# Kernel tuning notes

Measured on AMD Instinct MI355X. Metric: run time of the kernel, lower is better.

## Reference

```python
import jax, jax.numpy as jnp
import numpy as np

C = 64
C2 = C // 2


def conv1x1(x, w, b):
    # x: [B,Cin,H,W], w: [Cout,Cin], b: [Cout]
    return jnp.einsum('bchw,oc->bohw', x, w) + b[None, :, None, None]


def maxpool2(x):
    # 2x2 max pool, stride 2. x: [B,C,H,W] -> [B,C,H//2,W//2]
    B, Ch, H, W = x.shape
    x = x.reshape(B, Ch, H // 2, 2, W // 2, 2)
    return x.max(axis=(3, 5))


def setup_inputs() -> dict:
    key = jax.random.key(0)
    ks = jax.random.split(key, 9)
    B, H, W = 4, 128, 128
    x = jax.random.normal(ks[0], (B, C, H, W), dtype=jnp.float32)
    s_in = 1.0 / np.sqrt(C)
    s_mid = 1.0 / np.sqrt(C2)
    return {
        'x': x,
        'w_theta': jax.random.uniform(ks[1], (C2, C), jnp.float32, -s_in, s_in),
        'b_theta': jax.random.uniform(ks[2], (C2,), jnp.float32, -s_in, s_in),
        'w_phi': jax.random.uniform(ks[3], (C2, C), jnp.float32, -s_in, s_in),
        'b_phi': jax.random.uniform(ks[4], (C2,), jnp.float32, -s_in, s_in),
        'w_g': jax.random.uniform(ks[5], (C2, C), jnp.float32, -s_in, s_in),
        'b_g': jax.random.uniform(ks[6], (C2,), jnp.float32, -s_in, s_in),
        'w_out': jax.random.uniform(ks[7], (C, C2), jnp.float32, -s_mid, s_mid),
        'b_out': jax.random.uniform(ks[8], (C,), jnp.float32, -s_mid, s_mid),
    }


def reference(x, w_theta, b_theta, w_phi, b_phi, w_g, b_g, w_out, b_out):
    B, Ch, H, W = x.shape
    theta = conv1x1(x, w_theta, b_theta)            # [B,C2,H,W]
    phi = maxpool2(conv1x1(x, w_phi, b_phi))        # [B,C2,H/2,W/2]
    g = maxpool2(conv1x1(x, w_g, b_g))              # [B,C2,H/2,W/2]

    theta_flat = theta.reshape(B, C2, H * W).transpose(0, 2, 1)   # [B,HW,C2]
    phi_flat = phi.reshape(B, C2, -1)                              # [B,C2,hw4]
    g_flat = g.reshape(B, C2, -1).transpose(0, 2, 1)               # [B,hw4,C2]

    attn = jnp.einsum('bnc,bcm->bnm', theta_flat, phi_flat)       # [B,HW,hw4]
    attn = jax.nn.softmax(attn, axis=-1)
    y = jnp.einsum('bnm,bmc->bnc', attn, g_flat)                   # [B,HW,C2]
    y = y.transpose(0, 2, 1).reshape(B, C2, H, W)
    return conv1x1(y, w_out, b_out) + x
```

## Files before the change

kernel.cpp:

```cpp
#include <hip/hip_runtime.h>

#define HW    16384
#define Wh    128
#define Cin   64
#define C2    32
#define HW4   4096

typedef short short8 __attribute__((ext_vector_type(8)));
typedef float float4v __attribute__((ext_vector_type(4)));
typedef unsigned uint4v __attribute__((ext_vector_type(4)));

#define LOG2E 1.44269504f
#define OFFE  43.2808512f

__device__ __forceinline__ unsigned pack2bf16(float lo, float hi) {
  unsigned ul = __builtin_bit_cast(unsigned, lo);
  unsigned uh = __builtin_bit_cast(unsigned, hi);
  ul = (ul + 0x7fffu + ((ul >> 16) & 1u)) >> 16;
  uh = (uh + 0x7fffu + ((uh >> 16) & 1u)) & 0xffff0000u;
  return ul | uh;
}
__device__ __forceinline__ unsigned short f2bf(float f) {
  unsigned u = __builtin_bit_cast(unsigned, f);
  return (unsigned short)((u + 0x7fffu + ((u >> 16) & 1u)) >> 16);
}
__device__ __forceinline__ unsigned packtrunc(float lo, float hi) {
  return __builtin_amdgcn_perm(__builtin_bit_cast(unsigned, hi),
                               __builtin_bit_cast(unsigned, lo), 0x07060302u);
}

__global__ __launch_bounds__(256) void repack_w_kern(
    const float* __restrict__ wt, const float* __restrict__ bt,
    const float* __restrict__ wp, const float* __restrict__ bp,
    const float* __restrict__ wg, const float* __restrict__ bg,
    float* __restrict__ wAll, float* __restrict__ bAll) {
  int idx = blockIdx.x * 256 + threadIdx.x;
  if (idx < 6144) {
    int og = idx / 1536, rem = idx % 1536;
    int c = rem / 24, j = rem % 24;
    int o = og * 8 + (j & 7);
    float v;
    if (j < 8)       v = wt[o * Cin + c] * LOG2E;
    else if (j < 16) v = wp[o * Cin + c];
    else             v = wg[o * Cin + c];
    wAll[idx] = v;
  } else if (idx < 6240) {
    int i2 = idx - 6144;
    int og = i2 / 24, j = i2 % 24;
    int o = og * 8 + (j & 7);
    bAll[i2] = (j < 8) ? bt[o] * LOG2E : (j < 16 ? bp[o] : bg[o]);
  }
}

__global__ __launch_bounds__(256) void conv_qkv_kern(
    const float* __restrict__ x, const float* __restrict__ wAll,
    const float* __restrict__ bAll, unsigned short* __restrict__ Q,
    unsigned short* __restrict__ K, unsigned short* __restrict__ Vt) {
  __shared__ float smX[2][8][256];
  __shared__ unsigned short smV[8][64];
  int tid = threadIdx.x;
  int og = blockIdx.y, bz = blockIdx.z;
  int pxbase = blockIdx.x * 2 * Wh;
  int jloc = tid >> 2;
  int rpar = (tid >> 1) & 1, cpar = tid & 1;
  int myPx = rpar * Wh + 2 * jloc + cpar;
  const float* xb = x + (size_t)bz * Cin * HW + pxbase;
  const float* wc = wAll + og * 1536;
  const float* bb = bAll + og * 24;

  auto stage = [&](int cb8, int buf) {
#pragma unroll
    for (int u = 0; u < 2; ++u) {
      int f = u * 256 + tid;
      int ch = f >> 6, p4 = f & 63;
      *(float4*)&smX[buf][ch][p4 * 4] =
          *(const float4*)(xb + (size_t)(cb8 * 8 + ch) * HW + p4 * 4);
    }
  };

  float acc[24];
#pragma unroll
  for (int k = 0; k < 24; ++k) acc[k] = bb[k];

  stage(0, 0);
  __syncthreads();
  for (int cb8 = 0; cb8 < 8; ++cb8) {
    if (cb8 < 7) stage(cb8 + 1, (cb8 + 1) & 1);
    float xv[8];
#pragma unroll
    for (int u = 0; u < 8; ++u) xv[u] = smX[cb8 & 1][u][myPx];
#pragma unroll
    for (int u = 0; u < 8; ++u) {
#pragma unroll
      for (int k = 0; k < 24; ++k)
        acc[k] = fmaf(wc[(cb8 * 8 + u) * 24 + k], xv[u], acc[k]);
    }
    __syncthreads();
  }

  int pp = blockIdx.x * 64 + jloc;
  int p = pxbase + myPx;
  {
    uint4 up;
    up.x = pack2bf16(acc[0], acc[1]); up.y = pack2bf16(acc[2], acc[3]);
    up.z = pack2bf16(acc[4], acc[5]); up.w = pack2bf16(acc[6], acc[7]);
    *(uint4*)(Q + ((size_t)bz * HW + p) * C2 + og * 8) = up;
  }
  float aP[8], aG[8];
#pragma unroll
  for (int o = 0; o < 8; ++o) {
    float vp = acc[8 + o], vg = acc[16 + o];
    vp = fmaxf(vp, __shfl_xor(vp, 1)); vp = fmaxf(vp, __shfl_xor(vp, 2));
    vg = fmaxf(vg, __shfl_xor(vg, 1)); vg = fmaxf(vg, __shfl_xor(vg, 2));
    aP[o] = vp; aG[o] = vg;
  }
  if ((tid & 3) == 0) {
    int loc = pp & 31, tile = pp >> 5;
    int prow = ((loc & 4) << 2) + ((loc >> 3) << 2) + (loc & 3);
    uint4 up;
    up.x = pack2bf16(aP[0], aP[1]); up.y = pack2bf16(aP[2], aP[3]);
    up.z = pack2bf16(aP[4], aP[5]); up.w = pack2bf16(aP[6], aP[7]);
    *(uint4*)(K + ((size_t)bz * HW4 + tile * 32 + prow) * C2 + og * 8) = up;
#pragma unroll
    for (int o = 0; o < 8; ++o) smV[o][tid >> 2] = f2bf(aG[o]);
  }
  __syncthreads();
  {
    int ch = tid >> 5, idx = tid & 31;
    unsigned v = ((unsigned*)smV)[ch * 32 + idx];
    *(unsigned*)(Vt + (size_t)bz * C2 * HW4 + (size_t)(og * 8 + ch) * HW4 +
                 blockIdx.x * 64 + 2 * idx) = v;
  }
}

__global__ __launch_bounds__(256, 4) void attn_mfma_kern(
    const unsigned short* __restrict__ Qb, const unsigned short* __restrict__ Kb,
    const unsigned short* __restrict__ Vt, const float* __restrict__ x,
    const float* __restrict__ w_out, const float* __restrict__ b_out,
    float* __restrict__ out) {
  __shared__ float smY[3][64][33];
  __shared__ float smL[4][64];
  int lane = threadIdx.x & 63;
  int wv = threadIdx.x >> 6;
  int quad = lane >> 4, l16 = lane & 15;
  int bz = blockIdx.y;
  int qrow0 = blockIdx.x * 64;

  short8 qf[4];
#pragma unroll
  for (int f = 0; f < 4; ++f)
    qf[f] = *(const short8*)(Qb + ((size_t)bz * HW + qrow0 + f * 16 + l16) * C2 + quad * 8);
  const unsigned short* kb = Kb + ((size_t)bz * HW4 + wv * 1024) * C2;
  const unsigned short* vb = Vt + (size_t)bz * C2 * HW4 + wv * 1024;

  short8 ones;
#pragma unroll
  for (int i = 0; i < 8; ++i) ones[i] = (short)0x3F80;

  float4v z = {0.f, 0.f, 0.f, 0.f};
  float4v ya[4] = {z, z, z, z};
  float4v yh[4] = {z, z, z, z};
  float4v y2[4] = {z, z, z, z};
  float4v moff = {-OFFE, -OFFE, -OFFE, -OFFE};

  for (int t = 0; t < 32; ++t) {
    const unsigned short* kt = kb + (size_t)t * 32 * C2;
    const unsigned short* vt = vb + t * 32;
    short8 ka = *(const short8*)(kt + (size_t)l16 * C2 + quad * 8);
    short8 kh = *(const short8*)(kt + (size_t)(16 + l16) * C2 + quad * 8);
    short8 va = *(const short8*)(vt + (size_t)l16 * HW4 + quad * 8);
    short8 vh = *(const short8*)(vt + (size_t)(16 + l16) * HW4 + quad * 8);
#pragma unroll
    for (int f = 0; f < 4; ++f) {
      float4v sa = __builtin_amdgcn_mfma_f32_16x16x32_bf16(ka, qf[f], moff, 0, 0, 0);
      float4v sh = __builtin_amdgcn_mfma_f32_16x16x32_bf16(kh, qf[f], moff, 0, 0, 0);
      float e0 = __builtin_amdgcn_exp2f(sa[0]), e1 = __builtin_amdgcn_exp2f(sa[1]);
      float e2 = __builtin_amdgcn_exp2f(sa[2]), e3 = __builtin_amdgcn_exp2f(sa[3]);
      float g0 = __builtin_amdgcn_exp2f(sh[0]), g1 = __builtin_amdgcn_exp2f(sh[1]);
      float g2 = __builtin_amdgcn_exp2f(sh[2]), g3 = __builtin_amdgcn_exp2f(sh[3]);
      uint4v d = {packtrunc(e0, e1), packtrunc(e2, e3),
                  packtrunc(g0, g1), packtrunc(g2, g3)};
      short8 pf = __builtin_bit_cast(short8, d);
      ya[f] = __builtin_amdgcn_mfma_f32_16x16x32_bf16(pf, va,   ya[f], 0, 0, 0);
      yh[f] = __builtin_amdgcn_mfma_f32_16x16x32_bf16(pf, vh,   yh[f], 0, 0, 0);
      y2[f] = __builtin_amdgcn_mfma_f32_16x16x32_bf16(pf, ones, y2[f], 0, 0, 0);
    }
  }

  if (l16 == 0) {
#pragma unroll
    for (int f = 0; f < 4; ++f)
#pragma unroll
      for (int r = 0; r < 4; ++r)
        smL[wv][f * 16 + quad * 4 + r] = y2[f][r];
  }
  if (wv > 0) {
    int pi = wv - 1;
#pragma unroll
    for (int f = 0; f < 4; ++f)
#pragma unroll
      for (int r = 0; r < 4; ++r) {
        int lr = f * 16 + quad * 4 + r;
        smY[pi][lr][l16] = ya[f][r];
        smY[pi][lr][16 + l16] = yh[f][r];
      }
  }
  __syncthreads();
  if (wv == 0) {
#pragma unroll
    for (int f = 0; f < 4; ++f)
#pragma unroll
      for (int r = 0; r < 4; ++r) {
        int lr = f * 16 + quad * 4 + r;
        float a0 = ya[f][r] + smY[0][lr][l16] + smY[1][lr][l16] + smY[2][lr][l16];
        float a1 = yh[f][r] + smY[0][lr][16 + l16] + smY[1][lr][16 + l16] + smY[2][lr][16 + l16];
        float L = smL[0][lr] + smL[1][lr] + smL[2][lr] + smL[3][lr];
        float inv = 1.f / L;
        smY[0][lr][l16] = a0 * inv;
        smY[0][lr][16 + l16] = a1 * inv;
      }
  }
  __syncthreads();

  {
    int px = lane;
    float yv[C2];
#pragma unroll
    for (int c = 0; c < C2; ++c) yv[c] = smY[0][px][c];
    const float* xb = x + (size_t)bz * Cin * HW + qrow0 + px;
    float* ob = out + (size_t)bz * Cin * HW + qrow0 + px;
#pragma unroll
    for (int i = 0; i < 16; ++i) {
      int co = wv * 16 + i;
      float s = b_out[co];
#pragma unroll
      for (int o = 0; o < C2; ++o) s = fmaf(w_out[co * C2 + o], yv[o], s);
      ob[(size_t)co * HW] = s + xb[(size_t)co * HW];
    }
  }
}

extern "C" void kernel_launch(void* const* d_in, const int* in_sizes, int n_in,
                              void* d_out, int out_size, void* d_ws, size_t ws_size,
                              hipStream_t stream) {
  const float* x       = (const float*)d_in[0];
  const float* w_theta = (const float*)d_in[1];
  const float* b_theta = (const float*)d_in[2];
  const float* w_phi   = (const float*)d_in[3];
  const float* b_phi   = (const float*)d_in[4];
  const float* w_g     = (const float*)d_in[5];
  const float* b_g     = (const float*)d_in[6];
  const float* w_out   = (const float*)d_in[7];
  const float* b_out   = (const float*)d_in[8];
  float* out = (float*)d_out;

  float* Yws = (float*)d_ws;
  unsigned short* Qb = (unsigned short*)(Yws + (size_t)4 * HW * C2);
  unsigned short* Kb = Qb + (size_t)4 * HW * C2;
  unsigned short* Vt = Kb + (size_t)4 * HW4 * C2;
  float* wAll = (float*)(Vt + (size_t)4 * HW4 * C2);
  float* bAll = wAll + 6144;

  repack_w_kern<<<25, 256, 0, stream>>>(w_theta, b_theta, w_phi, b_phi,
                                        w_g, b_g, wAll, bAll);
  conv_qkv_kern<<<dim3(64, 4, 4), 256, 0, stream>>>(x, wAll, bAll, Qb, Kb, Vt);
  attn_mfma_kern<<<dim3(HW / 64, 4), 256, 0, stream>>>(Qb, Kb, Vt, x,
                                                       w_out, b_out, out);
}
```

Baseline: 164.9 us.

## Load conv input directly from global and do maxpool via shared-memory reduction

```diff
diff --git a/kernel.cpp b/kernel.cpp
--- a/kernel.cpp
+++ b/kernel.cpp
@@ -56,65 +56,49 @@
     const float* __restrict__ x, const float* __restrict__ wAll,
     const float* __restrict__ bAll, unsigned short* __restrict__ Q,
     unsigned short* __restrict__ K, unsigned short* __restrict__ Vt) {
-  __shared__ float smX[2][8][256];
+  __shared__ float smP[256][17];
   __shared__ unsigned short smV[8][64];
   int tid = threadIdx.x;
   int og = blockIdx.y, bz = blockIdx.z;
   int pxbase = blockIdx.x * 2 * Wh;
-  int jloc = tid >> 2;
-  int rpar = (tid >> 1) & 1, cpar = tid & 1;
-  int myPx = rpar * Wh + 2 * jloc + cpar;
-  const float* xb = x + (size_t)bz * Cin * HW + pxbase;
+  const float* xb = x + (size_t)bz * Cin * HW + pxbase + tid;
   const float* wc = wAll + og * 1536;
   const float* bb = bAll + og * 24;
 
-  auto stage = [&](int cb8, int buf) {
-#pragma unroll
-    for (int u = 0; u < 2; ++u) {
-      int f = u * 256 + tid;
-      int ch = f >> 6, p4 = f & 63;
-      *(float4*)&smX[buf][ch][p4 * 4] =
-          *(const float4*)(xb + (size_t)(cb8 * 8 + ch) * HW + p4 * 4);
-    }
-  };
-
   float acc[24];
 #pragma unroll
   for (int k = 0; k < 24; ++k) acc[k] = bb[k];
 
-  stage(0, 0);
-  __syncthreads();
-  for (int cb8 = 0; cb8 < 8; ++cb8) {
-    if (cb8 < 7) stage(cb8 + 1, (cb8 + 1) & 1);
-    float xv[8];
-#pragma unroll
-    for (int u = 0; u < 8; ++u) xv[u] = smX[cb8 & 1][u][myPx];
-#pragma unroll
-    for (int u = 0; u < 8; ++u) {
-#pragma unroll
-      for (int k = 0; k < 24; ++k)
-        acc[k] = fmaf(wc[(cb8 * 8 + u) * 24 + k], xv[u], acc[k]);
-    }
-    __syncthreads();
-  }
-
-  int pp = blockIdx.x * 64 + jloc;
-  int p = pxbase + myPx;
+#pragma unroll
+  for (int ch = 0; ch < Cin; ++ch) {
+    float xv = xb[(size_t)ch * HW];
+#pragma unroll
+    for (int k = 0; k < 24; ++k)
+      acc[k] = fmaf(wc[ch * 24 + k], xv, acc[k]);
+  }
+
+  int p = pxbase + tid;
   {
     uint4 up;
     up.x = pack2bf16(acc[0], acc[1]); up.y = pack2bf16(acc[2], acc[3]);
     up.z = pack2bf16(acc[4], acc[5]); up.w = pack2bf16(acc[6], acc[7]);
     *(uint4*)(Q + ((size_t)bz * HW + p) * C2 + og * 8) = up;
   }
-  float aP[8], aG[8];
-#pragma unroll
-  for (int o = 0; o < 8; ++o) {
-    float vp = acc[8 + o], vg = acc[16 + o];
-    vp = fmaxf(vp, __shfl_xor(vp, 1)); vp = fmaxf(vp, __shfl_xor(vp, 2));
-    vg = fmaxf(vg, __shfl_xor(vg, 1)); vg = fmaxf(vg, __shfl_xor(vg, 2));
-    aP[o] = vp; aG[o] = vg;
-  }
-  if ((tid & 3) == 0) {
+#pragma unroll
+  for (int o = 0; o < 16; ++o) smP[tid][o] = acc[8 + o];
+  __syncthreads();
+
+  if (tid < 64) {
+    int j = tid;
+    float aP[8], aG[8];
+#pragma unroll
+    for (int o = 0; o < 8; ++o) {
+      aP[o] = fmaxf(fmaxf(smP[2 * j][o],       smP[2 * j + 1][o]),
+                    fmaxf(smP[128 + 2 * j][o], smP[129 + 2 * j][o]));
+      aG[o] = fmaxf(fmaxf(smP[2 * j][8 + o],       smP[2 * j + 1][8 + o]),
+                    fmaxf(smP[128 + 2 * j][8 + o], smP[129 + 2 * j][8 + o]));
+    }
+    int pp = blockIdx.x * 64 + j;
     int loc = pp & 31, tile = pp >> 5;
     int prow = ((loc & 4) << 2) + ((loc >> 3) << 2) + (loc & 3);
     uint4 up;
@@ -122,7 +106,7 @@
     up.z = pack2bf16(aP[4], aP[5]); up.w = pack2bf16(aP[6], aP[7]);
     *(uint4*)(K + ((size_t)bz * HW4 + tile * 32 + prow) * C2 + og * 8) = up;
 #pragma unroll
-    for (int o = 0; o < 8; ++o) smV[o][tid >> 2] = f2bf(aG[o]);
+    for (int o = 0; o < 8; ++o) smV[o][j] = f2bf(aG[o]);
   }
   __syncthreads();
   {
```

New measurement: 176.7 us. 1.07x slower.
